# Optimization experiments

Measured on AMD Instinct MI355X. Metric: run time of the kernel, lower is better.

## Reference

```python
import jax, jax.numpy as jnp
import numpy as np

B = 16          # patients
V = 30          # max_visit
NV = 1501       # num_nodes + 1 (node vocab incl. padding)
NE = 2001       # num_edges + 1 (relation vocab incl. padding)
H = 128         # hidden_dim
D = 128         # start_embed_dim
L = 2           # gnn layers
OUT = 25        # out_dim
N_TOTAL = 100000  # concatenated graph nodes
E = 800000        # concatenated graph edges
DECAY = 0.01
EPS = 0.0       # self_attn


def setup_inputs() -> dict:
    key = jax.random.key(0)
    ks = jax.random.split(key, 16)
    s = 0.02
    return dict(
        node_emb_w=jax.random.normal(ks[0], (NV, D), jnp.float32) * s,
        edge_emb_w=jax.random.normal(ks[1], (NE, D), jnp.float32) * s,
        lin_w=jax.random.normal(ks[2], (H, D), jnp.float32) * s,
        lin_b=jnp.zeros((H,), jnp.float32),
        alpha_w=jax.random.normal(ks[3], (L, NV, NV), jnp.float32) * 0.01,
        alpha_b=jnp.zeros((L, NV), jnp.float32),
        beta_w=jax.random.normal(ks[4], (L, 1, NV), jnp.float32) * 0.01,
        beta_b=jnp.zeros((L, 1), jnp.float32),
        wr_w=jax.random.normal(ks[5], (L, 1, H), jnp.float32) * s,
        wr_b=jnp.zeros((L, 1), jnp.float32),
        conv_w=jax.random.normal(ks[6], (L, H, H), jnp.float32) * s,
        conv_b=jnp.zeros((L, H), jnp.float32),
        mlp_w=jax.random.normal(ks[7], (OUT, 2 * H), jnp.float32) * s,
        mlp_b=jnp.zeros((OUT,), jnp.float32),
        visit_node=jax.random.randint(ks[8], (B, V, NV), 0, 2).astype(jnp.int32),
        ehr_nodes=jax.random.randint(ks[9], (B, NV), 0, 2).astype(jnp.int32),
        cat_node_ids=jax.random.randint(ks[10], (N_TOTAL,), 1, NV).astype(jnp.int32),
        cat_edge_ids=jax.random.randint(ks[11], (E,), 1, NE).astype(jnp.int32),
        edge_index=jax.random.randint(ks[12], (2, E), 0, N_TOTAL).astype(jnp.int32),
        batch=jnp.repeat(jnp.arange(B, dtype=jnp.int32), N_TOTAL // B),
    )


def reference(node_emb_w, edge_emb_w, lin_w, lin_b, alpha_w, alpha_b,
              beta_w, beta_b, wr_w, wr_b, conv_w, conv_b, mlp_w, mlp_b,
              visit_node, ehr_nodes, cat_node_ids, cat_edge_ids, edge_index, batch):
    # lambda_j = exp(decay * (max_visit - j)), shape [1, V, 1]
    lam = jnp.exp(DECAY * (V - jnp.arange(V, dtype=jnp.float32)))[None, :, None]
    # embedding lookup + shared linear projection
    x = node_emb_w[cat_node_ids] @ lin_w.T + lin_b          # [N_total, H]
    eattr = edge_emb_w[cat_edge_ids] @ lin_w.T + lin_b      # [E, H]
    vn = visit_node.astype(jnp.float32)                     # [B, V, NV]
    src, dst = edge_index[0], edge_index[1]
    xj_nid = cat_node_ids[src]                               # [E]
    xj_b = batch[src]                                        # [E]
    for l in range(L):
        # visit-level attention: softmax over visits (dim=1)
        alpha = jax.nn.softmax(vn @ alpha_w[l].T + alpha_b[l], axis=1)   # [B,V,NV]
        beta = jnp.tanh(vn @ beta_w[l].T + beta_b[l]) * lam              # [B,V,1]
        attn = jnp.sum(alpha * beta, axis=1)                              # [B,NV]
        e_attn = attn[xj_b, xj_nid][:, None]                              # [E,1] per-edge gather
        # BiAttentionGNNConv: message = relu(x_j * attn * sigmoid(W_R e)), aggr=add
        w_rel = jax.nn.sigmoid(eattr @ wr_w[l].T + wr_b[l])               # [E,1]
        msg = jax.nn.relu(x[src] * e_attn * w_rel)                        # [E,H]
        agg = jax.ops.segment_sum(msg, dst, num_segments=N_TOTAL)        # scatter-add
        x = jax.nn.relu((agg + (1.0 + EPS) * x) @ conv_w[l].T + conv_b[l])
    # global mean pool over batch segments
    counts = jax.ops.segment_sum(jnp.ones((N_TOTAL,), jnp.float32), batch, num_segments=B)
    x_graph = jax.ops.segment_sum(x, batch, num_segments=B) / counts[:, None]
    # node branch: multi-hot average of node embeddings, then shared lin
    ehr = ehr_nodes.astype(jnp.float32)
    x_node = (ehr @ node_emb_w) / jnp.sum(ehr, axis=1, keepdims=True)
    x_node = x_node @ lin_w.T + lin_b
    return jnp.concatenate([x_graph, x_node], axis=1) @ mlp_w.T + mlp_b  # [B, OUT]
```

## Files before the change

kernel.cpp:

```cpp
#include <hip/hip_runtime.h>
#include <math.h>

namespace {
constexpr int kB = 16, kV = 30, kNV = 1501, kNE = 2001, kH = 128, kD = 128,
              kL = 2, kOut = 25, kNT = 100000, kE = 800000, kM = kB * kV;
constexpr int kNB = (kNT + 255) / 256;
constexpr int kKP = 1504;
constexpr int kKSZ = 4;
constexpr int kNVZ = 1536;
constexpr int kMZ = 512;
}

typedef __attribute__((ext_vector_type(8))) short bfrag;
typedef __attribute__((ext_vector_type(4))) float ffrag;

__device__ inline unsigned short f2bf(float x) {
  unsigned u = __float_as_uint(x);
  unsigned r = u + 0x7FFFu + ((u >> 16) & 1u);
  return (unsigned short)(r >> 16);
}
__device__ inline float bf2f(unsigned short h) {
  return __uint_as_float(((unsigned)h) << 16);
}

__global__ void pn_kernel(const float* __restrict__ emb, const float* __restrict__ lw,
                          const float* __restrict__ lb, const float* __restrict__ cw,
                          const float* __restrict__ cb, float* __restrict__ pn,
                          float* __restrict__ pq2, float* __restrict__ ps) {
  int n = blockIdx.x, h = threadIdx.x;
  __shared__ float erow[kD];
  __shared__ float row[kD];
  erow[h] = emb[(size_t)n * kD + h];
  __syncthreads();
  float acc = lb[h];
#pragma unroll 8
  for (int d = 0; d < kD; d++) acc += erow[d] * lw[h * kD + d];
  pn[(size_t)n * kH + h] = acc;
  row[h] = acc;
  __syncthreads();
  float ap = 0.f, am = 0.f, aps = cb[h];
  const float* wr = cw + h * kD;
#pragma unroll 8
  for (int d = 0; d < kD; d++) {
    float r = row[d];
    float w = wr[d];
    ap = fmaf(fmaxf(r, 0.f), w, ap);
    am = fmaf(fmaxf(-r, 0.f), w, am);
    aps = fmaf(r, w, aps);
  }
  pq2[(size_t)n * kH + h] = ap;
  pq2[(size_t)(kNV + n) * kH + h] = am;
  ps[(size_t)n * kH + h] = aps;
}

__global__ void xnode_kernel(const int* __restrict__ ehr, const float* __restrict__ pn,
                             float* __restrict__ xacc, int* __restrict__ cnte) {
  int b = blockIdx.x;
  int c = blockIdx.y;
  int h = threadIdx.x;
  int n0 = c * 128;
  __shared__ int flags[128];
  int gn = n0 + h;
  flags[h] = (gn < kNV) ? ehr[(size_t)b * kNV + gn] : 0;
  __syncthreads();
  float acc = 0.f;
  int cnt = 0;
  int n1 = min(n0 + 128, kNV);
  for (int n = n0; n < n1; ++n) {
    if (flags[n - n0]) {
      acc += pn[(size_t)n * kH + h];
      cnt++;
    }
  }
  atomicAdd(&xacc[b * kH + h], acc);
  if (h == 0) atomicAdd(&cnte[b], cnt);
}

__global__ void uc_kernel(const float* __restrict__ wrw, const float* __restrict__ wrb,
                          const float* __restrict__ lw, const float* __restrict__ lb,
                          float* __restrict__ uc) {
  int t = threadIdx.x;
  int l = t >> 7, d = t & 127;
  float s = 0.f;
  for (int h = 0; h < kH; h++) s += wrw[l * kH + h] * lw[h * kD + d];
  uc[t] = s;
  if (t < kL) {
    float c = wrb[t];
    for (int h = 0; h < kH; h++) c += wrw[t * kH + h] * lb[h];
    uc[256 + t] = c;
  }
}

__global__ void wrel_kernel(const float* __restrict__ eemb, const float* __restrict__ uc,
                            float* __restrict__ wrel) {
  int idx = blockIdx.x * blockDim.x + threadIdx.x;
  if (idx >= kL * kNE) return;
  int l = idx / kNE, r = idx % kNE;
  float z = uc[256 + l];
  const float* u = uc + l * 128;
  const float* er = eemb + (size_t)r * kD;
  for (int d = 0; d < kD; d++) z += er[d] * u[d];
  wrel[idx] = 1.f / (1.f + expf(-z));
}

__global__ void beta_kernel(const int* __restrict__ vn, const float* __restrict__ bw,
                            const float* __restrict__ bb, float* __restrict__ beta) {
  int blk = blockIdx.x;
  int l = blk / kM, r = blk % kM;
  int v = r % kV;
  int lane = threadIdx.x;
  const int* row = vn + (size_t)r * kNV;
  const float* w = bw + (size_t)l * kNV;
  float s = 0.f;
  for (int k = lane; k < kNV; k += 64) s += (float)row[k] * w[k];
  for (int off = 32; off > 0; off >>= 1) s += __shfl_down(s, off, 64);
  if (lane == 0) {
    float lam = expf(0.01f * (float)(kV - v));
    beta[blk] = tanhf(s + bb[l]) * lam;
  }
}

__global__ void vnbf_kernel(const int* __restrict__ vn, short* __restrict__ out) {
  int m = blockIdx.x;
  int b = m >> 5, v = m & 31;
  for (int k = threadIdx.x; k < kKP; k += 256) {
    int val = (v < kV && k < kNV) ? vn[((size_t)(b * kV + v)) * kNV + k] : 0;
    out[(size_t)m * kKP + k] = val ? (short)0x3F80 : (short)0;
  }
}

__global__ void awsplit_kernel(const float* __restrict__ aw, short* __restrict__ awh) {
  int n = blockIdx.x;
  int l = blockIdx.y;
  const size_t pl = (size_t)kKP * kKP;
  size_t rowo = ((size_t)l * kKP + n) * kKP;
  for (int k = threadIdx.x; k < kKP; k += 256) {
    float x = (n < kNV && k < kNV) ? aw[((size_t)l * kNV + n) * kNV + k] : 0.f;
    unsigned short h1 = f2bf(x);
    float r1 = x - bf2f(h1);
    unsigned short h2 = f2bf(r1);
    float r2 = r1 - bf2f(h2);
    unsigned short h3 = f2bf(r2);
    awh[rowo + k] = (short)h1;
    awh[2 * pl + rowo + k] = (short)h2;
    awh[4 * pl + rowo + k] = (short)h3;
  }
}

__global__ void zmfma_kernel(const short* __restrict__ vnbf, const short* __restrict__ awh,
                             float* __restrict__ zp) {
  const int l = blockIdx.z >> 2, ks = blockIdx.z & 3;
  const int wv = threadIdx.x >> 6, lane = threadIdx.x & 63;
  const int m0 = (blockIdx.y * 4 + wv) * 64;
  const int n0 = blockIdx.x * 32;
  const int lrow = lane & 15;
  const int koff = (lane >> 4) * 8;
  const size_t pl = (size_t)kKP * kKP;
  const short* b0p = awh + (size_t)l * pl;
  const short* b1p = awh + (2 + (size_t)l) * 2 * pl / 2;
  const short* p0 = awh + ((size_t)0 * 2 + l) * pl;
  const short* p1 = awh + ((size_t)1 * 2 + l) * pl;
  const short* p2 = awh + ((size_t)2 * 2 + l) * pl;
  (void)b0p; (void)b1p;
  ffrag acc[4][2];
#pragma unroll
  for (int i = 0; i < 4; ++i)
#pragma unroll
    for (int j = 0; j < 2; ++j) acc[i][j] = ffrag{0.f, 0.f, 0.f, 0.f};
  const int ct0 = ks * 12;
  const int ct1 = min(ct0 + 12, 47);
  for (int kt = ct0; kt < ct1; ++kt) {
    const int k = kt * 32 + koff;
    bfrag a0 = *(const bfrag*)(vnbf + (size_t)(m0 + 0 * 16 + lrow) * kKP + k);
    bfrag a1 = *(const bfrag*)(vnbf + (size_t)(m0 + 1 * 16 + lrow) * kKP + k);
    bfrag a2 = *(const bfrag*)(vnbf + (size_t)(m0 + 2 * 16 + lrow) * kKP + k);
    bfrag a3 = *(const bfrag*)(vnbf + (size_t)(m0 + 3 * 16 + lrow) * kKP + k);
    {
      bfrag b0 = *(const bfrag*)(p0 + (size_t)(n0 + lrow) * kKP + k);
      bfrag b1 = *(const bfrag*)(p0 + (size_t)(n0 + 16 + lrow) * kKP + k);
      acc[0][0] = __builtin_amdgcn_mfma_f32_16x16x32_bf16(a0, b0, acc[0][0], 0, 0, 0);
      acc[1][0] = __builtin_amdgcn_mfma_f32_16x16x32_bf16(a1, b0, acc[1][0], 0, 0, 0);
      acc[2][0] = __builtin_amdgcn_mfma_f32_16x16x32_bf16(a2, b0, acc[2][0], 0, 0, 0);
      acc[3][0] = __builtin_amdgcn_mfma_f32_16x16x32_bf16(a3, b0, acc[3][0], 0, 0, 0);
      acc[0][1] = __builtin_amdgcn_mfma_f32_16x16x32_bf16(a0, b1, acc[0][1], 0, 0, 0);
      acc[1][1] = __builtin_amdgcn_mfma_f32_16x16x32_bf16(a1, b1, acc[1][1], 0, 0, 0);
      acc[2][1] = __builtin_amdgcn_mfma_f32_16x16x32_bf16(a2, b1, acc[2][1], 0, 0, 0);
      acc[3][1] = __builtin_amdgcn_mfma_f32_16x16x32_bf16(a3, b1, acc[3][1], 0, 0, 0);
    }
    {
      bfrag b0 = *(const bfrag*)(p1 + (size_t)(n0 + lrow) * kKP + k);
      bfrag b1 = *(const bfrag*)(p1 + (size_t)(n0 + 16 + lrow) * kKP + k);
      acc[0][0] = __builtin_amdgcn_mfma_f32_16x16x32_bf16(a0, b0, acc[0][0], 0, 0, 0);
      acc[1][0] = __builtin_amdgcn_mfma_f32_16x16x32_bf16(a1, b0, acc[1][0], 0, 0, 0);
      acc[2][0] = __builtin_amdgcn_mfma_f32_16x16x32_bf16(a2, b0, acc[2][0], 0, 0, 0);
      acc[3][0] = __builtin_amdgcn_mfma_f32_16x16x32_bf16(a3, b0, acc[3][0], 0, 0, 0);
      acc[0][1] = __builtin_amdgcn_mfma_f32_16x16x32_bf16(a0, b1, acc[0][1], 0, 0, 0);
      acc[1][1] = __builtin_amdgcn_mfma_f32_16x16x32_bf16(a1, b1, acc[1][1], 0, 0, 0);
      acc[2][1] = __builtin_amdgcn_mfma_f32_16x16x32_bf16(a2, b1, acc[2][1], 0, 0, 0);
      acc[3][1] = __builtin_amdgcn_mfma_f32_16x16x32_bf16(a3, b1, acc[3][1], 0, 0, 0);
    }
    {
      bfrag b0 = *(const bfrag*)(p2 + (size_t)(n0 + lrow) * kKP + k);
      bfrag b1 = *(const bfrag*)(p2 + (size_t)(n0 + 16 + lrow) * kKP + k);
      acc[0][0] = __builtin_amdgcn_mfma_f32_16x16x32_bf16(a0, b0, acc[0][0], 0, 0, 0);
      acc[1][0] = __builtin_amdgcn_mfma_f32_16x16x32_bf16(a1, b0, acc[1][0], 0, 0, 0);
      acc[2][0] = __builtin_amdgcn_mfma_f32_16x16x32_bf16(a2, b0, acc[2][0], 0, 0, 0);
      acc[3][0] = __builtin_amdgcn_mfma_f32_16x16x32_bf16(a3, b0, acc[3][0], 0, 0, 0);
      acc[0][1] = __builtin_amdgcn_mfma_f32_16x16x32_bf16(a0, b1, acc[0][1], 0, 0, 0);
      acc[1][1] = __builtin_amdgcn_mfma_f32_16x16x32_bf16(a1, b1, acc[1][1], 0, 0, 0);
      acc[2][1] = __builtin_amdgcn_mfma_f32_16x16x32_bf16(a2, b1, acc[2][1], 0, 0, 0);
      acc[3][1] = __builtin_amdgcn_mfma_f32_16x16x32_bf16(a3, b1, acc[3][1], 0, 0, 0);
    }
  }
  const int drow0 = (lane >> 4) * 4;
  float* zb = zp + (size_t)(ks * kL + l) * kMZ * kNVZ;
#pragma unroll
  for (int i = 0; i < 4; ++i) {
    int mrow = m0 + i * 16 + drow0;
#pragma unroll
    for (int j = 0; j < 2; ++j) {
      int ncol = n0 + j * 16 + lrow;
#pragma unroll
      for (int r = 0; r < 4; ++r) zb[(size_t)(mrow + r) * kNVZ + ncol] = acc[i][j][r];
    }
  }
}

__global__ void zsm_kernel(const float* __restrict__ zp, const float* __restrict__ beta,
                           float* __restrict__ attn) {
  int idx = blockIdx.x * blockDim.x + threadIdx.x;
  if (idx >= kL * kB * kNV) return;
  int n = idx % kNV;
  int lb_ = idx / kNV;
  int l = lb_ / kB, b = lb_ % kB;
  const size_t PSTR = (size_t)kL * kMZ * kNVZ;
  const float* p = zp + ((size_t)l * kMZ + b * 32) * kNVZ + n;
  float zz[kV];
  float m = -1e30f;
#pragma unroll
  for (int v = 0; v < kV; ++v) {
    size_t o = (size_t)v * kNVZ;
    float s = p[o] + p[o + PSTR] + p[o + 2 * PSTR] + p[o + 3 * PSTR];
    zz[v] = s;
    m = fmaxf(m, s);
  }
  float s = 0.f, num = 0.f;
  const float* bet = beta + lb_ * kV;
#pragma unroll
  for (int v = 0; v < kV; ++v) {
    float e = expf(zz[v] - m);
    s += e;
    num += e * bet[v];
  }
  attn[idx] = num / s;
}

__global__ void hist_kernel(const int* __restrict__ ei, const int* __restrict__ nid,
                            const int* __restrict__ batch, const float* __restrict__ attn,
                            int* __restrict__ deg, int* __restrict__ deg2) {
  int e = blockIdx.x * blockDim.x + threadIdx.x;
  if (e >= kE) return;
  int d = ei[kE + e];
  atomicAdd(&deg[d], 1);
  int s = ei[e];
  float a1 = attn[(size_t)kB * kNV + batch[s] * kNV + nid[s]];
  if (a1 > 0.f) atomicAdd(&deg2[d], 1);
}

__global__ void scan1_dual(const int* __restrict__ deg, const int* __restrict__ deg2,
                           int* __restrict__ off, int* __restrict__ off2,
                           int* __restrict__ part, int* __restrict__ part2) {
  int t = threadIdx.x, i = blockIdx.x * 256 + t;
  int v1 = (i < kNT) ? deg[i] : 0;
  int v2 = (i < kNT) ? deg2[i] : 0;
  __shared__ int s1[256];
  __shared__ int s2[256];
  s1[t] = v1;
  s2[t] = v2;
  __syncthreads();
  for (int o = 1; o < 256; o <<= 1) {
    int x1 = (t >= o) ? s1[t - o] : 0;
    int x2 = (t >= o) ? s2[t - o] : 0;
    __syncthreads();
    s1[t] += x1;
    s2[t] += x2;
    __syncthreads();
  }
  if (i < kNT) {
    off[i] = s1[t] - v1;
    off2[i] = s2[t] - v2;
  }
  if (t == 255) {
    part[blockIdx.x] = s1[255];
    part2[blockIdx.x] = s2[255];
  }
}

__global__ void scan2_dual(int* __restrict__ part, int* __restrict__ part2) {
  int t = threadIdx.x;
  int v1 = (t < kNB) ? part[t] : 0;
  int v2 = (t < kNB) ? part2[t] : 0;
  __shared__ int s1[512];
  __shared__ int s2[512];
  s1[t] = v1;
  s2[t] = v2;
  __syncthreads();
  for (int o = 1; o < 512; o <<= 1) {
    int x1 = (t >= o) ? s1[t - o] : 0;
    int x2 = (t >= o) ? s2[t - o] : 0;
    __syncthreads();
    s1[t] += x1;
    s2[t] += x2;
    __syncthreads();
  }
  if (t < kNB) {
    part[t] = s1[t] - v1;
    part2[t] = s2[t] - v2;
  }
}

__global__ void scan3_dual(int* __restrict__ off, const int* __restrict__ part,
                           int* __restrict__ cursor, int* __restrict__ off2,
                           const int* __restrict__ part2, int* __restrict__ cursor2) {
  int i = blockIdx.x * 256 + threadIdx.x;
  if (i >= kNT) return;
  int o1 = off[i] + part[blockIdx.x];
  off[i] = o1;
  cursor[i] = o1;
  int o2 = off2[i] + part2[blockIdx.x];
  off2[i] = o2;
  cursor2[i] = o2;
}

__global__ void cnt_kernel(const int* __restrict__ batch, int* __restrict__ cnt) {
  __shared__ int hist[kB];
  int t = threadIdx.x;
  if (t < kB) hist[t] = 0;
  __syncthreads();
  int i = blockIdx.x * blockDim.x + t;
  if (i < kNT) atomicAdd(&hist[batch[i]], 1);
  __syncthreads();
  if (t < kB && hist[t]) atomicAdd(&cnt[t], hist[t]);
}

__global__ void scatter_kernel(const int* __restrict__ ei, const int* __restrict__ nid,
                               const int* __restrict__ eid, const int* __restrict__ batch,
                               const float* __restrict__ attn, const float* __restrict__ wrel,
                               int* __restrict__ cursor, int* __restrict__ csn,
                               float* __restrict__ cs0, int* __restrict__ cursor2,
                               int* __restrict__ csrc2, float* __restrict__ cs1c) {
  int e = blockIdx.x * blockDim.x + threadIdx.x;
  if (e >= kE) return;
  int s = ei[e], d = ei[kE + e];
  int b = batch[s], n = nid[s], r = eid[e];
  float a0 = attn[(size_t)b * kNV + n];
  float a1 = attn[(size_t)kB * kNV + b * kNV + n];
  float w0 = wrel[r], w1 = wrel[kNE + r];
  int pos = atomicAdd(&cursor[d], 1);
  csn[pos] = n + ((a0 > 0.f) ? 0 : kNV);
  cs0[pos] = fabsf(a0) * w0;
  if (a1 > 0.f) {
    int p2 = atomicAdd(&cursor2[d], 1);
    csrc2[p2] = s;
    cs1c[p2] = a1 * w1;
  }
}

#define GACC(A, V, C)                                  \
  A.x = fmaf(V.x, C, A.x); A.y = fmaf(V.y, C, A.y);    \
  A.z = fmaf(V.z, C, A.z); A.w = fmaf(V.w, C, A.w);

__global__ void l1_kernel(const float* __restrict__ pq2, const float* __restrict__ psTab,
                          const int* __restrict__ nid, const int* __restrict__ csn,
                          const float* __restrict__ cs0, const int* __restrict__ off,
                          const int* __restrict__ endv, float* __restrict__ xa) {
  const int tid = threadIdx.x;
  const int lane = tid & 63;
  const int sub = lane >> 5, sl = lane & 31;
  const int hw = (tid >> 6) * 2 + sub;
  int node = blockIdx.x * 16 + hw;
  if (node >= kNT) return;
  const float4* x4 = (const float4*)pq2;
  float4 a0 = ((const float4*)psTab)[(size_t)nid[node] * 32 + sl];
  float4 a1 = {0.f, 0.f, 0.f, 0.f};
  float4 a2 = {0.f, 0.f, 0.f, 0.f};
  float4 a3 = {0.f, 0.f, 0.f, 0.f};
  int j0 = off[node], j1 = endv[node];
  for (int base = j0; base < j1; base += 32) {
    int n = j1 - base;
    if (n > 32) n = 32;
    int sidx = 0;
    float ssc = 0.f;
    if (sl < n) {
      sidx = csn[base + sl];
      ssc = cs0[base + sl];
    }
    int t = 0;
    for (; t + 8 <= n; t += 8) {
      int s0 = __shfl(sidx, sub * 32 + t + 0, 64);
      int s1 = __shfl(sidx, sub * 32 + t + 1, 64);
      int s2 = __shfl(sidx, sub * 32 + t + 2, 64);
      int s3 = __shfl(sidx, sub * 32 + t + 3, 64);
      int s4i = __shfl(sidx, sub * 32 + t + 4, 64);
      int s5 = __shfl(sidx, sub * 32 + t + 5, 64);
      int s6 = __shfl(sidx, sub * 32 + t + 6, 64);
      int s7 = __shfl(sidx, sub * 32 + t + 7, 64);
      float c0 = __shfl(ssc, sub * 32 + t + 0, 64);
      float c1 = __shfl(ssc, sub * 32 + t + 1, 64);
      float c2 = __shfl(ssc, sub * 32 + t + 2, 64);
      float c3 = __shfl(ssc, sub * 32 + t + 3, 64);
      float c4 = __shfl(ssc, sub * 32 + t + 4, 64);
      float c5 = __shfl(ssc, sub * 32 + t + 5, 64);
      float c6 = __shfl(ssc, sub * 32 + t + 6, 64);
      float c7 = __shfl(ssc, sub * 32 + t + 7, 64);
      float4 v0 = x4[(size_t)s0 * 32 + sl];
      float4 v1 = x4[(size_t)s1 * 32 + sl];
      float4 v2 = x4[(size_t)s2 * 32 + sl];
      float4 v3 = x4[(size_t)s3 * 32 + sl];
      float4 v4 = x4[(size_t)s4i * 32 + sl];
      float4 v5 = x4[(size_t)s5 * 32 + sl];
      float4 v6 = x4[(size_t)s6 * 32 + sl];
      float4 v7 = x4[(size_t)s7 * 32 + sl];
      GACC(a0, v0, c0);
      GACC(a1, v1, c1);
      GACC(a2, v2, c2);
      GACC(a3, v3, c3);
      GACC(a0, v4, c4);
      GACC(a1, v5, c5);
      GACC(a2, v6, c6);
      GACC(a3, v7, c7);
    }
    for (; t + 4 <= n; t += 4) {
      int s0 = __shfl(sidx, sub * 32 + t + 0, 64);
      int s1 = __shfl(sidx, sub * 32 + t + 1, 64);
      int s2 = __shfl(sidx, sub * 32 + t + 2, 64);
      int s3 = __shfl(sidx, sub * 32 + t + 3, 64);
      float c0 = __shfl(ssc, sub * 32 + t + 0, 64);
      float c1 = __shfl(ssc, sub * 32 + t + 1, 64);
      float c2 = __shfl(ssc, sub * 32 + t + 2, 64);
      float c3 = __shfl(ssc, sub * 32 + t + 3, 64);
      float4 v0 = x4[(size_t)s0 * 32 + sl];
      float4 v1 = x4[(size_t)s1 * 32 + sl];
      float4 v2 = x4[(size_t)s2 * 32 + sl];
      float4 v3 = x4[(size_t)s3 * 32 + sl];
      GACC(a0, v0, c0);
      GACC(a1, v1, c1);
      GACC(a2, v2, c2);
      GACC(a3, v3, c3);
    }
    for (; t < n; ++t) {
      int s = __shfl(sidx, sub * 32 + t, 64);
      float sc = __shfl(ssc, sub * 32 + t, 64);
      float4 xv = x4[(size_t)s * 32 + sl];
      GACC(a0, xv, sc);
    }
  }
  float4 o;
  o.x = fmaxf(a0.x + a1.x + a2.x + a3.x, 0.f);
  o.y = fmaxf(a0.y + a1.y + a2.y + a3.y, 0.f);
  o.z = fmaxf(a0.z + a1.z + a2.z + a3.z, 0.f);
  o.w = fmaxf(a0.w + a1.w + a2.w + a3.w, 0.f);
  ((float4*)xa)[(size_t)node * 32 + sl] = o;
}

template <int POOL>
__global__ void gconv_kernel(const float* __restrict__ srcTab,
                             const float* __restrict__ selfTab,
                             const int* __restrict__ cidx, const float* __restrict__ cscal,
                             const int* __restrict__ off, const int* __restrict__ endv,
                             const int* __restrict__ selfIdx, const float* __restrict__ w,
                             const float* __restrict__ bias, float* __restrict__ xout,
                             float* __restrict__ xg, const int* __restrict__ batch) {
  const int nb = blockIdx.x * 64;
  const int tid = threadIdx.x;
  __shared__ float As[128 * 64];
  __shared__ float Ws[32 * 132];
  const int wv = tid >> 6;
  const int lane = tid & 63;
  const int sub = lane >> 5, sl = lane & 31;
  const int hw = wv * 2 + sub;
  const float4* x4 = (const float4*)srcTab;
  const float4* s4 = (const float4*)selfTab;
  for (int p = 0; p < 4; ++p) {
    int nl = p * 16 + hw;
    int node = nb + nl;
    if (node < kNT) {
      int selfRow = selfIdx ? selfIdx[node] : node;
      float4 a0 = s4[(size_t)selfRow * 32 + sl];
      float4 a1 = {0.f, 0.f, 0.f, 0.f};
      float4 a2 = {0.f, 0.f, 0.f, 0.f};
      float4 a3 = {0.f, 0.f, 0.f, 0.f};
      int j0 = off[node], j1 = endv[node];
      for (int base = j0; base < j1; base += 32) {
        int n = j1 - base;
        if (n > 32) n = 32;
        int sidx = 0;
        float ssc = 0.f;
        if (sl < n) {
          sidx = cidx[base + sl];
          ssc = cscal[base + sl];
        }
        int t = 0;
        for (; t + 8 <= n; t += 8) {
          int s0 = __shfl(sidx, sub * 32 + t + 0, 64);
          int s1 = __shfl(sidx, sub * 32 + t + 1, 64);
          int s2 = __shfl(sidx, sub * 32 + t + 2, 64);
          int s3 = __shfl(sidx, sub * 32 + t + 3, 64);
          int s4i = __shfl(sidx, sub * 32 + t + 4, 64);
          int s5 = __shfl(sidx, sub * 32 + t + 5, 64);
          int s6 = __shfl(sidx, sub * 32 + t + 6, 64);
          int s7 = __shfl(sidx, sub * 32 + t + 7, 64);
          float c0 = __shfl(ssc, sub * 32 + t + 0, 64);
          float c1 = __shfl(ssc, sub * 32 + t + 1, 64);
          float c2 = __shfl(ssc, sub * 32 + t + 2, 64);
          float c3 = __shfl(ssc, sub * 32 + t + 3, 64);
          float c4 = __shfl(ssc, sub * 32 + t + 4, 64);
          float c5 = __shfl(ssc, sub * 32 + t + 5, 64);
          float c6 = __shfl(ssc, sub * 32 + t + 6, 64);
          float c7 = __shfl(ssc, sub * 32 + t + 7, 64);
          float4 v0 = x4[(size_t)s0 * 32 + sl];
          float4 v1 = x4[(size_t)s1 * 32 + sl];
          float4 v2 = x4[(size_t)s2 * 32 + sl];
          float4 v3 = x4[(size_t)s3 * 32 + sl];
          float4 v4 = x4[(size_t)s4i * 32 + sl];
          float4 v5 = x4[(size_t)s5 * 32 + sl];
          float4 v6 = x4[(size_t)s6 * 32 + sl];
          float4 v7 = x4[(size_t)s7 * 32 + sl];
          GACC(a0, v0, c0);
          GACC(a1, v1, c1);
          GACC(a2, v2, c2);
          GACC(a3, v3, c3);
          GACC(a0, v4, c4);
          GACC(a1, v5, c5);
          GACC(a2, v6, c6);
          GACC(a3, v7, c7);
        }
        for (; t + 4 <= n; t += 4) {
          int s0 = __shfl(sidx, sub * 32 + t + 0, 64);
          int s1 = __shfl(sidx, sub * 32 + t + 1, 64);
          int s2 = __shfl(sidx, sub * 32 + t + 2, 64);
          int s3 = __shfl(sidx, sub * 32 + t + 3, 64);
          float c0 = __shfl(ssc, sub * 32 + t + 0, 64);
          float c1 = __shfl(ssc, sub * 32 + t + 1, 64);
          float c2 = __shfl(ssc, sub * 32 + t + 2, 64);
          float c3 = __shfl(ssc, sub * 32 + t + 3, 64);
          float4 v0 = x4[(size_t)s0 * 32 + sl];
          float4 v1 = x4[(size_t)s1 * 32 + sl];
          float4 v2 = x4[(size_t)s2 * 32 + sl];
          float4 v3 = x4[(size_t)s3 * 32 + sl];
          GACC(a0, v0, c0);
          GACC(a1, v1, c1);
          GACC(a2, v2, c2);
          GACC(a3, v3, c3);
        }
        for (; t < n; ++t) {
          int s = __shfl(sidx, sub * 32 + t, 64);
          float sc = __shfl(ssc, sub * 32 + t, 64);
          float4 xv = x4[(size_t)s * 32 + sl];
          GACC(a0, xv, sc);
        }
      }
      float av[4] = {a0.x + a1.x + a2.x + a3.x, a0.y + a1.y + a2.y + a3.y,
                     a0.z + a1.z + a2.z + a3.z, a0.w + a1.w + a2.w + a3.w};
#pragma unroll
      for (int j = 0; j < 4; ++j) {
        int d = sl * 4 + j;
        int g = (nl >> 2) ^ (sl & 15);
        As[d * 64 + (g << 2) + (nl & 3)] = av[j];
      }
    }
  }
  __syncthreads();
  const int tx = tid & 31, ty = tid >> 5;
  const int n0 = tx * 4;
  float acc[4][4] = {};
  for (int kc = 0; kc < 4; ++kc) {
    if (kc) __syncthreads();
#pragma unroll
    for (int i = 0; i < 2; ++i) {
      int fi = tid + i * 512;
      int hh = fi >> 3, c4 = (fi & 7) * 4;
      float4 v = *(const float4*)(w + (size_t)hh * kD + kc * 32 + c4);
      Ws[(c4 + 0) * 132 + hh] = v.x;
      Ws[(c4 + 1) * 132 + hh] = v.y;
      Ws[(c4 + 2) * 132 + hh] = v.z;
      Ws[(c4 + 3) * 132 + hh] = v.w;
    }
    __syncthreads();
#pragma unroll
    for (int dd = 0; dd < 32; ++dd) {
      int d = kc * 32 + dd;
      float4 a = *(const float4*)&As[d * 64 + ((ty ^ ((d >> 2) & 15)) << 2)];
      float4 b0 = *(const float4*)&Ws[dd * 132 + n0];
      float am[4] = {a.x, a.y, a.z, a.w};
      float bn[4] = {b0.x, b0.y, b0.z, b0.w};
#pragma unroll
      for (int i2 = 0; i2 < 4; ++i2)
#pragma unroll
        for (int j2 = 0; j2 < 4; ++j2) acc[i2][j2] += am[i2] * bn[j2];
    }
  }
  float4 bv0 = *(const float4*)(bias + n0);
  float bb[4] = {bv0.x, bv0.y, bv0.z, bv0.w};
  if (POOL == 0) {
#pragma unroll
    for (int i2 = 0; i2 < 4; ++i2) {
      int r = nb + ty * 4 + i2;
      if (r < kNT) {
        float4 o0;
        o0.x = fmaxf(acc[i2][0] + bb[0], 0.f);
        o0.y = fmaxf(acc[i2][1] + bb[1], 0.f);
        o0.z = fmaxf(acc[i2][2] + bb[2], 0.f);
        o0.w = fmaxf(acc[i2][3] + bb[3], 0.f);
        *(float4*)(xout + (size_t)r * kH + n0) = o0;
      }
    }
  } else {
    int rlast = min(nb + 63, kNT - 1);
    int b0 = batch[nb], b1 = batch[rlast];
    if (b0 == b1) {
      float p[4] = {};
#pragma unroll
      for (int i2 = 0; i2 < 4; ++i2) {
        int r = nb + ty * 4 + i2;
        if (r < kNT) {
#pragma unroll
          for (int j2 = 0; j2 < 4; ++j2) p[j2] += fmaxf(acc[i2][j2] + bb[j2], 0.f);
        }
      }
      __syncthreads();
      float* Ls = Ws;
#pragma unroll
      for (int j2 = 0; j2 < 4; ++j2) Ls[ty * 132 + n0 + j2] = p[j2];
      __syncthreads();
      if (tid < 128) {
        float s = 0.f;
#pragma unroll
        for (int r2 = 0; r2 < 16; ++r2) s += Ls[r2 * 132 + tid];
        atomicAdd(&xg[b0 * kH + tid], s);
      }
    } else {
#pragma unroll
      for (int i2 = 0; i2 < 4; ++i2) {
        int r = nb + ty * 4 + i2;
        if (r < kNT) {
          int br = batch[r];
#pragma unroll
          for (int j2 = 0; j2 < 4; ++j2)
            atomicAdd(&xg[br * kH + n0 + j2], fmaxf(acc[i2][j2] + bb[j2], 0.f));
        }
      }
    }
  }
}

__global__ void final_kernel(const float* __restrict__ xg, const int* __restrict__ cnt,
                             const float* __restrict__ xacc, const int* __restrict__ cnte,
                             const float* __restrict__ mw, const float* __restrict__ mb,
                             float* __restrict__ out) {
  int idx = blockIdx.x * blockDim.x + threadIdx.x;
  if (idx >= kB * kOut) return;
  int b = idx / kOut, o = idx % kOut;
  float invg = 1.f / (float)cnt[b];
  float invn = 1.f / (float)cnte[b];
  float acc = mb[o];
  const float* w = mw + (size_t)o * (2 * kH);
  for (int h = 0; h < kH; h++) acc += xg[b * kH + h] * invg * w[h];
  for (int h = 0; h < kH; h++) acc += xacc[b * kH + h] * invn * w[kH + h];
  out[idx] = acc;
}

extern "C" void kernel_launch(void* const* d_in, const int* in_sizes, int n_in,
                              void* d_out, int out_size, void* d_ws, size_t ws_size,
                              hipStream_t stream) {
  const float* node_emb = (const float*)d_in[0];
  const float* edge_emb = (const float*)d_in[1];
  const float* lin_w = (const float*)d_in[2];
  const float* lin_b = (const float*)d_in[3];
  const float* alpha_w = (const float*)d_in[4];
  const float* alpha_b = (const float*)d_in[5];
  const float* beta_w = (const float*)d_in[6];
  const float* beta_b = (const float*)d_in[7];
  const float* wr_w = (const float*)d_in[8];
  const float* wr_b = (const float*)d_in[9];
  const float* conv_w = (const float*)d_in[10];
  const float* conv_b = (const float*)d_in[11];
  const float* mlp_w = (const float*)d_in[12];
  const float* mlp_b = (const float*)d_in[13];
  const int* visit_node = (const int*)d_in[14];
  const int* ehr_nodes = (const int*)d_in[15];
  const int* cat_node_ids = (const int*)d_in[16];
  const int* cat_edge_ids = (const int*)d_in[17];
  const int* edge_index = (const int*)d_in[18];
  const int* batch = (const int*)d_in[19];

  char* ws = (char*)d_ws;
  float* ZP = (float*)(ws);
  float* XA = (float*)(ws);
  float* PN = (float*)(ws + 51200000);
  short* VNBF = (short*)(ws + 52100000);
  short* AWH = (short*)(ws + 54000000);
  int* CSN = (int*)(ws + 54000000);
  int* CSRS2 = (int*)(ws + 57200000);
  float* CS1C = (float*)(ws + 60400000);
  int* OFF2 = (int*)(ws + 63600000);
  float* PQ2 = (float*)(ws + 81200000);
  float* PS = (float*)(ws + 82800000);
  float* ATTN = (float*)(ws + 102400000);
  float* BETA = (float*)(ws + 102592256);
  float* UC = (float*)(ws + 102596352);
  float* WREL = (float*)(ws + 102597632);
  int* OFF = (int*)(ws + 102613760);
  int* CURSOR = (int*)(ws + 103014016);
  int* CURSOR2 = (int*)(ws + 103414016);
  int* SPART = (int*)(ws + 103814016);
  int* SPART2 = (int*)(ws + 103816064);
  float* CS0 = (float*)(ws + 106616064);
  float* XG = (float*)(ws + 113016064);
  int* CNT = (int*)(ws + 113024256);
  float* XNACC = (float*)(ws + 113024320);
  int* CNTE = (int*)(ws + 113032512);

  pn_kernel<<<kNV, kH, 0, stream>>>(node_emb, lin_w, lin_b, conv_w, conv_b, PN, PQ2, PS);
  hipMemsetAsync(XG, 0, 16512, stream);
  xnode_kernel<<<dim3(kB, 12), kH, 0, stream>>>(ehr_nodes, PN, XNACC, CNTE);
  cnt_kernel<<<kNB, 256, 0, stream>>>(batch, CNT);
  uc_kernel<<<1, 256, 0, stream>>>(wr_w, wr_b, lin_w, lin_b, UC);
  wrel_kernel<<<(kL * kNE + 255) / 256, 256, 0, stream>>>(edge_emb, UC, WREL);
  beta_kernel<<<kL * kM, 64, 0, stream>>>(visit_node, beta_w, beta_b, BETA);
  vnbf_kernel<<<kMZ, 256, 0, stream>>>(visit_node, VNBF);
  awsplit_kernel<<<dim3(kKP, kL), 256, 0, stream>>>(alpha_w, AWH);
  zmfma_kernel<<<dim3(47, 2, kL * kKSZ), 256, 0, stream>>>(VNBF, AWH, ZP);
  zsm_kernel<<<(kL * kB * kNV + 255) / 256, 256, 0, stream>>>(ZP, BETA, ATTN);

  hipMemsetAsync(CURSOR, 0, 800000, stream);
  hist_kernel<<<(kE + 255) / 256, 256, 0, stream>>>(edge_index, cat_node_ids, batch, ATTN,
                                                    CURSOR, CURSOR2);
  scan1_dual<<<kNB, 256, 0, stream>>>(CURSOR, CURSOR2, OFF, OFF2, SPART, SPART2);
  scan2_dual<<<1, 512, 0, stream>>>(SPART, SPART2);
  scan3_dual<<<kNB, 256, 0, stream>>>(OFF, SPART, CURSOR, OFF2, SPART2, CURSOR2);
  scatter_kernel<<<(kE + 255) / 256, 256, 0, stream>>>(edge_index, cat_node_ids, cat_edge_ids,
                                                       batch, ATTN, WREL, CURSOR, CSN, CS0,
                                                       CURSOR2, CSRS2, CS1C);

  l1_kernel<<<(kNT + 15) / 16, 512, 0, stream>>>(PQ2, PS, cat_node_ids, CSN, CS0, OFF,
                                                 CURSOR, XA);
  gconv_kernel<1><<<(kNT + 63) / 64, 512, 0, stream>>>(XA, XA, CSRS2, CS1C, OFF2, CURSOR2,
                                                       nullptr, conv_w + (size_t)kH * kD,
                                                       conv_b + kH, nullptr, XG, batch);

  final_kernel<<<2, 256, 0, stream>>>(XG, CNT, XNACC, CNTE, mlp_w, mlp_b, (float*)d_out);
}
```

Before: 352.2 us.

## Run layer-2 conv GEMM on bf16x3 MFMA instead of FP32 FMA

Replaces the FP32 scalar-FMA 64x128x128 GEMM in gconv_kernel with MFMA 16x16x32 bf16 instructions. Both operands are split three ways into bf16 to keep near-FP32 accuracy, and conv weights are pre-split by a new wsplit_kernel. The aggregated activations are stored in LDS as three swizzled bf16 planes, and the pooled epilogue is reworked around the MFMA accumulator layout. The aim is to cut the ALU time of the fused gather-GEMM-pool kernel, at the cost of six MFMAs per tile, an extra small launch, and slightly different rounding.

```diff
diff --git a/kernel.cpp b/kernel.cpp
--- a/kernel.cpp
+++ b/kernel.cpp
@@ -147,6 +147,20 @@
   }
 }
 
+__global__ void wsplit_kernel(const float* __restrict__ w, short* __restrict__ wbf) {
+  int h = blockIdx.x;
+  int d = threadIdx.x;
+  float x = w[(size_t)h * kD + d];
+  unsigned short h1 = f2bf(x);
+  float r1 = x - bf2f(h1);
+  unsigned short h2 = f2bf(r1);
+  float r2 = r1 - bf2f(h2);
+  unsigned short h3 = f2bf(r2);
+  wbf[h * 128 + d] = (short)h1;
+  wbf[16384 + h * 128 + d] = (short)h2;
+  wbf[32768 + h * 128 + d] = (short)h3;
+}
+
 __global__ void zmfma_kernel(const short* __restrict__ vnbf, const short* __restrict__ awh,
                              float* __restrict__ zp) {
   const int l = blockIdx.z >> 2, ks = blockIdx.z & 3;
@@ -156,12 +170,9 @@
   const int lrow = lane & 15;
   const int koff = (lane >> 4) * 8;
   const size_t pl = (size_t)kKP * kKP;
-  const short* b0p = awh + (size_t)l * pl;
-  const short* b1p = awh + (2 + (size_t)l) * 2 * pl / 2;
   const short* p0 = awh + ((size_t)0 * 2 + l) * pl;
   const short* p1 = awh + ((size_t)1 * 2 + l) * pl;
   const short* p2 = awh + ((size_t)2 * 2 + l) * pl;
-  (void)b0p; (void)b1p;
   ffrag acc[4][2];
 #pragma unroll
   for (int i = 0; i < 4; ++i)
@@ -463,30 +474,25 @@
   ((float4*)xa)[(size_t)node * 32 + sl] = o;
 }
 
-template <int POOL>
-__global__ void gconv_kernel(const float* __restrict__ srcTab,
-                             const float* __restrict__ selfTab,
-                             const int* __restrict__ cidx, const float* __restrict__ cscal,
-                             const int* __restrict__ off, const int* __restrict__ endv,
-                             const int* __restrict__ selfIdx, const float* __restrict__ w,
-                             const float* __restrict__ bias, float* __restrict__ xout,
-                             float* __restrict__ xg, const int* __restrict__ batch) {
+__global__ void gconv_kernel(const float* __restrict__ srcTab, const int* __restrict__ cidx,
+                             const float* __restrict__ cscal, const int* __restrict__ off,
+                             const int* __restrict__ endv, const short* __restrict__ wbf,
+                             const float* __restrict__ bias, float* __restrict__ xg,
+                             const int* __restrict__ batch) {
   const int nb = blockIdx.x * 64;
   const int tid = threadIdx.x;
-  __shared__ float As[128 * 64];
-  __shared__ float Ws[32 * 132];
+  __shared__ short AsBF[3 * 64 * 128];
   const int wv = tid >> 6;
   const int lane = tid & 63;
   const int sub = lane >> 5, sl = lane & 31;
   const int hw = wv * 2 + sub;
   const float4* x4 = (const float4*)srcTab;
-  const float4* s4 = (const float4*)selfTab;
   for (int p = 0; p < 4; ++p) {
     int nl = p * 16 + hw;
     int node = nb + nl;
+    float av[4] = {0.f, 0.f, 0.f, 0.f};
     if (node < kNT) {
-      int selfRow = selfIdx ? selfIdx[node] : node;
-      float4 a0 = s4[(size_t)selfRow * 32 + sl];
+      float4 a0 = x4[(size_t)node * 32 + sl];
       float4 a1 = {0.f, 0.f, 0.f, 0.f};
       float4 a2 = {0.f, 0.f, 0.f, 0.f};
       float4 a3 = {0.f, 0.f, 0.f, 0.f};
@@ -560,95 +566,99 @@
           GACC(a0, xv, sc);
         }
       }
-      float av[4] = {a0.x + a1.x + a2.x + a3.x, a0.y + a1.y + a2.y + a3.y,
-                     a0.z + a1.z + a2.z + a3.z, a0.w + a1.w + a2.w + a3.w};
-#pragma unroll
-      for (int j = 0; j < 4; ++j) {
-        int d = sl * 4 + j;
-        int g = (nl >> 2) ^ (sl & 15);
-        As[d * 64 + (g << 2) + (nl & 3)] = av[j];
+      av[0] = a0.x + a1.x + a2.x + a3.x;
+      av[1] = a0.y + a1.y + a2.y + a3.y;
+      av[2] = a0.z + a1.z + a2.z + a3.z;
+      av[3] = a0.w + a1.w + a2.w + a3.w;
+    }
+    short q0[4], q1[4], q2[4];
+#pragma unroll
+    for (int j = 0; j < 4; ++j) {
+      float x = av[j];
+      unsigned short h1 = f2bf(x);
+      float r1 = x - bf2f(h1);
+      unsigned short h2 = f2bf(r1);
+      float r2 = r1 - bf2f(h2);
+      unsigned short h3 = f2bf(r2);
+      q0[j] = (short)h1;
+      q1[j] = (short)h2;
+      q2[j] = (short)h3;
+    }
+    int basei = nl * 128 + (((sl >> 1) ^ (nl & 15)) << 3) + ((sl & 1) << 2);
+    *(short4*)&AsBF[basei] = *(short4*)q0;
+    *(short4*)&AsBF[8192 + basei] = *(short4*)q1;
+    *(short4*)&AsBF[16384 + basei] = *(short4*)q2;
+  }
+  __syncthreads();
+  const int mt = wv & 3, nh = wv >> 2;
+  const int m0 = mt * 16;
+  const int lrow = lane & 15;
+  const int lk = lane >> 4;
+  ffrag acc[4];
+#pragma unroll
+  for (int i = 0; i < 4; ++i) acc[i] = ffrag{0.f, 0.f, 0.f, 0.f};
+  for (int kc = 0; kc < 4; ++kc) {
+    int ga = (((kc * 4 + lk) ^ lrow) << 3);
+    int arow = (m0 + lrow) * 128;
+    bfrag a1 = *(const bfrag*)&AsBF[arow + ga];
+    bfrag a2 = *(const bfrag*)&AsBF[8192 + arow + ga];
+    bfrag a3 = *(const bfrag*)&AsBF[16384 + arow + ga];
+#pragma unroll
+    for (int nt = 0; nt < 4; ++nt) {
+      int h0 = nh * 64 + nt * 16;
+      const short* wb = wbf + (size_t)(h0 + lrow) * 128 + kc * 32 + lk * 8;
+      bfrag b1 = *(const bfrag*)(wb);
+      bfrag b2 = *(const bfrag*)(wb + 16384);
+      bfrag b3 = *(const bfrag*)(wb + 32768);
+      acc[nt] = __builtin_amdgcn_mfma_f32_16x16x32_bf16(a1, b1, acc[nt], 0, 0, 0);
+      acc[nt] = __builtin_amdgcn_mfma_f32_16x16x32_bf16(a1, b2, acc[nt], 0, 0, 0);
+      acc[nt] = __builtin_amdgcn_mfma_f32_16x16x32_bf16(a2, b1, acc[nt], 0, 0, 0);
+      acc[nt] = __builtin_amdgcn_mfma_f32_16x16x32_bf16(a1, b3, acc[nt], 0, 0, 0);
+      acc[nt] = __builtin_amdgcn_mfma_f32_16x16x32_bf16(a2, b2, acc[nt], 0, 0, 0);
+      acc[nt] = __builtin_amdgcn_mfma_f32_16x16x32_bf16(a3, b1, acc[nt], 0, 0, 0);
+    }
+  }
+  const int drow = lk * 4;
+  int rlast = min(nb + 63, kNT - 1);
+  int b0 = batch[nb], b1v = batch[rlast];
+  if (b0 == b1v) {
+    float tot[4];
+#pragma unroll
+    for (int nt = 0; nt < 4; ++nt) {
+      int hcol = nh * 64 + nt * 16 + lrow;
+      float bb = bias[hcol];
+      float s = 0.f;
+#pragma unroll
+      for (int r = 0; r < 4; ++r) {
+        int node = nb + m0 + drow + r;
+        float v = fmaxf(acc[nt][r] + bb, 0.f);
+        s += (node < kNT) ? v : 0.f;
       }
-    }
-  }
-  __syncthreads();
-  const int tx = tid & 31, ty = tid >> 5;
-  const int n0 = tx * 4;
-  float acc[4][4] = {};
-  for (int kc = 0; kc < 4; ++kc) {
-    if (kc) __syncthreads();
-#pragma unroll
-    for (int i = 0; i < 2; ++i) {
-      int fi = tid + i * 512;
-      int hh = fi >> 3, c4 = (fi & 7) * 4;
-      float4 v = *(const float4*)(w + (size_t)hh * kD + kc * 32 + c4);
-      Ws[(c4 + 0) * 132 + hh] = v.x;
-      Ws[(c4 + 1) * 132 + hh] = v.y;
-      Ws[(c4 + 2) * 132 + hh] = v.z;
-      Ws[(c4 + 3) * 132 + hh] = v.w;
+      s += __shfl_xor(s, 16, 64);
+      s += __shfl_xor(s, 32, 64);
+      tot[nt] = s;
     }
     __syncthreads();
-#pragma unroll
-    for (int dd = 0; dd < 32; ++dd) {
-      int d = kc * 32 + dd;
-      float4 a = *(const float4*)&As[d * 64 + ((ty ^ ((d >> 2) & 15)) << 2)];
-      float4 b0 = *(const float4*)&Ws[dd * 132 + n0];
-      float am[4] = {a.x, a.y, a.z, a.w};
-      float bn[4] = {b0.x, b0.y, b0.z, b0.w};
-#pragma unroll
-      for (int i2 = 0; i2 < 4; ++i2)
-#pragma unroll
-        for (int j2 = 0; j2 < 4; ++j2) acc[i2][j2] += am[i2] * bn[j2];
-    }
-  }
-  float4 bv0 = *(const float4*)(bias + n0);
-  float bb[4] = {bv0.x, bv0.y, bv0.z, bv0.w};
-  if (POOL == 0) {
-#pragma unroll
-    for (int i2 = 0; i2 < 4; ++i2) {
-      int r = nb + ty * 4 + i2;
-      if (r < kNT) {
-        float4 o0;
-        o0.x = fmaxf(acc[i2][0] + bb[0], 0.f);
-        o0.y = fmaxf(acc[i2][1] + bb[1], 0.f);
-        o0.z = fmaxf(acc[i2][2] + bb[2], 0.f);
-        o0.w = fmaxf(acc[i2][3] + bb[3], 0.f);
-        *(float4*)(xout + (size_t)r * kH + n0) = o0;
-      }
-    }
+    float* pool = (float*)AsBF;
+    if (tid < 128) pool[tid] = 0.f;
+    __syncthreads();
+    if (lk == 0) {
+#pragma unroll
+      for (int nt = 0; nt < 4; ++nt)
+        atomicAdd(&pool[nh * 64 + nt * 16 + lrow], tot[nt]);
+    }
+    __syncthreads();
+    if (tid < 128) atomicAdd(&xg[b0 * kH + tid], pool[tid]);
   } else {
-    int rlast = min(nb + 63, kNT - 1);
-    int b0 = batch[nb], b1 = batch[rlast];
-    if (b0 == b1) {
-      float p[4] = {};
-#pragma unroll
-      for (int i2 = 0; i2 < 4; ++i2) {
-        int r = nb + ty * 4 + i2;
-        if (r < kNT) {
-#pragma unroll
-          for (int j2 = 0; j2 < 4; ++j2) p[j2] += fmaxf(acc[i2][j2] + bb[j2], 0.f);
-        }
-      }
-      __syncthreads();
-      float* Ls = Ws;
-#pragma unroll
-      for (int j2 = 0; j2 < 4; ++j2) Ls[ty * 132 + n0 + j2] = p[j2];
-      __syncthreads();
-      if (tid < 128) {
-        float s = 0.f;
-#pragma unroll
-        for (int r2 = 0; r2 < 16; ++r2) s += Ls[r2 * 132 + tid];
-        atomicAdd(&xg[b0 * kH + tid], s);
-      }
-    } else {
-#pragma unroll
-      for (int i2 = 0; i2 < 4; ++i2) {
-        int r = nb + ty * 4 + i2;
-        if (r < kNT) {
-          int br = batch[r];
-#pragma unroll
-          for (int j2 = 0; j2 < 4; ++j2)
-            atomicAdd(&xg[br * kH + n0 + j2], fmaxf(acc[i2][j2] + bb[j2], 0.f));
-        }
+#pragma unroll
+    for (int nt = 0; nt < 4; ++nt) {
+      int hcol = nh * 64 + nt * 16 + lrow;
+      float bb = bias[hcol];
+#pragma unroll
+      for (int r = 0; r < 4; ++r) {
+        int node = nb + m0 + drow + r;
+        if (node < kNT)
+          atomicAdd(&xg[batch[node] * kH + hcol], fmaxf(acc[nt][r] + bb, 0.f));
       }
     }
   }
@@ -706,6 +716,7 @@
   int* OFF2 = (int*)(ws + 63600000);
   float* PQ2 = (float*)(ws + 81200000);
   float* PS = (float*)(ws + 82800000);
+  short* WBF = (short*)(ws + 96400000);
   float* ATTN = (float*)(ws + 102400000);
   float* BETA = (float*)(ws + 102592256);
   float* UC = (float*)(ws + 102596352);
@@ -730,6 +741,7 @@
   beta_kernel<<<kL * kM, 64, 0, stream>>>(visit_node, beta_w, beta_b, BETA);
   vnbf_kernel<<<kMZ, 256, 0, stream>>>(visit_node, VNBF);
   awsplit_kernel<<<dim3(kKP, kL), 256, 0, stream>>>(alpha_w, AWH);
+  wsplit_kernel<<<kH, kD, 0, stream>>>(conv_w + (size_t)kH * kD, WBF);
   zmfma_kernel<<<dim3(47, 2, kL * kKSZ), 256, 0, stream>>>(VNBF, AWH, ZP);
   zsm_kernel<<<(kL * kB * kNV + 255) / 256, 256, 0, stream>>>(ZP, BETA, ATTN);
 
@@ -745,9 +757,8 @@
 
   l1_kernel<<<(kNT + 15) / 16, 512, 0, stream>>>(PQ2, PS, cat_node_ids, CSN, CS0, OFF,
                                                  CURSOR, XA);
-  gconv_kernel<1><<<(kNT + 63) / 64, 512, 0, stream>>>(XA, XA, CSRS2, CS1C, OFF2, CURSOR2,
-                                                       nullptr, conv_w + (size_t)kH * kD,
-                                                       conv_b + kH, nullptr, XG, batch);
+  gconv_kernel<<<(kNT + 63) / 64, 512, 0, stream>>>(XA, CSRS2, CS1C, OFF2, CURSOR2, WBF,
+                                                    conv_b + kH, XG, batch);
 
   final_kernel<<<2, 256, 0, stream>>>(XG, CNT, XNACC, CNTE, mlp_w, mlp_b, (float*)d_out);
 }
```

New measurement: 384.9 us. 1.09x slower.
